# Performance work log

Hardware: AMD Instinct MI355X
Metric: run time of the kernel (lower is better)

The kernel has to match this reference:

```python
import jax, jax.numpy as jnp
import numpy as np

N, C, K, H = 131072, 512, 128, 8  # points, channels, patch_size, heads


def setup_inputs() -> dict:
    key = jax.random.key(0)
    ks = jax.random.split(key, 6)
    feat = jax.random.normal(ks[0], (N, C), dtype=jnp.float32)
    Wqkv = jax.random.normal(ks[1], (C, 3 * C), dtype=jnp.float32) * 0.02
    bqkv = jax.random.normal(ks[2], (3 * C,), dtype=jnp.float32) * 0.02
    Wproj = jax.random.normal(ks[3], (C, C), dtype=jnp.float32) * 0.02
    bproj = jax.random.normal(ks[4], (C,), dtype=jnp.float32) * 0.02
    order = jax.random.permutation(ks[5], N).astype(jnp.int64)  # serialized order (all clusters full)
    inverse = jnp.argsort(order).astype(jnp.int64)              # serialized inverse
    return {"feat": feat, "Wqkv": Wqkv, "bqkv": bqkv, "Wproj": Wproj,
            "bproj": bproj, "order": order, "inverse": inverse}


def reference(feat, Wqkv, bqkv, Wproj, bproj, order, inverse):
    hd = C // H
    scale = hd ** -0.5
    qkv = feat @ Wqkv + bqkv                 # [N, 3C]
    qkv = qkv[order]                         # gather by serialized order
    qkv = qkv.reshape(-1, K, 3, H, hd)       # [W, K, 3, H, hd]
    qkv = jnp.moveaxis(qkv, 2, 0)            # [3, W, K, H, hd]
    q = jnp.swapaxes(qkv[0], 1, 2)           # [W, H, K, hd]
    k = jnp.swapaxes(qkv[1], 1, 2)
    v = jnp.swapaxes(qkv[2], 1, 2)
    # upcast_attention / upcast_softmax -> compute scores & softmax in fp32
    attn = jnp.einsum('whkd,whjd->whkj', (q * scale).astype(jnp.float32),
                      k.astype(jnp.float32))             # [W, H, K, K]
    attn = jax.nn.softmax(attn, axis=-1).astype(feat.dtype)
    out = jnp.einsum('whkj,whjd->whkd', attn, v)          # [W, H, K, hd]
    out = jnp.swapaxes(out, 1, 2).reshape(-1, C)          # [N, C]
    out = out[inverse]                                    # scatter back via inverse
    out = out @ Wproj + bproj
    return out
```

## Files before the change

kernel.cpp:

```cpp
#include <hip/hip_runtime.h>
#include <hip/hip_bf16.h>
#include <cstdint>
#include <cstddef>

typedef __bf16 bf16;
typedef __bf16 bf16x8 __attribute__((ext_vector_type(8)));
typedef float f32x4 __attribute__((ext_vector_type(4)));

#define N_PTS 131072
#define CDIM  512
#define C3    1536
#define HD    64
#define NH    8
#define KWIN  128

static __device__ __forceinline__ bf16 cvt(float x) { return (bf16)x; }

static __device__ __forceinline__ void gld16(const bf16* g, bf16* l) {
    __builtin_amdgcn_global_load_lds(
        (const __attribute__((address_space(1))) void*)g,
        (__attribute__((address_space(3))) void*)l, 16, 0, 0);
}

__global__ __launch_bounds__(256) void k_prep(
    const float* __restrict__ Wqkv, const float* __restrict__ Wproj,
    bf16* __restrict__ Wqkv_t, bf16* __restrict__ Wproj_t)
{
    int idx = blockIdx.x * 256 + threadIdx.x;
    if (idx < CDIM * C3) {
        int k = idx / C3, c = idx % C3;
        Wqkv_t[(size_t)c * CDIM + k] = cvt(Wqkv[idx]);
    } else {
        int j = idx - CDIM * C3;
        if (j < CDIM * CDIM) {
            int k = j / CDIM, c = j % CDIM;
            Wproj_t[(size_t)c * CDIM + k] = cvt(Wproj[j]);
        }
    }
}

__global__ __launch_bounds__(256) void k_gather(
    const float* __restrict__ feat, const int* __restrict__ order,
    bf16* __restrict__ feat_g)
{
    int row = blockIdx.x * 2 + (threadIdx.x >> 7);
    int c   = (threadIdx.x & 127) << 2;
    int src = order[row];
    float4 v = *reinterpret_cast<const float4*>(feat + (size_t)src * CDIM + c);
    union { bf16 e[4]; uint2 u; } pk;
    pk.e[0] = cvt(v.x); pk.e[1] = cvt(v.y); pk.e[2] = cvt(v.z); pk.e[3] = cvt(v.w);
    *reinterpret_cast<uint2*>(feat_g + (size_t)row * CDIM + c) = pk.u;
}

template <bool F32OUT, int NT>
__global__ __launch_bounds__(512, 4) void k_gemm(
    const bf16* __restrict__ Ag, const bf16* __restrict__ Bt,
    const float* __restrict__ bias, void* __restrict__ outp)
{
    __shared__ __align__(16) bf16 As[2][128 * 32];
    __shared__ __align__(16) bf16 Bs[2][256 * 32];

    const int t    = threadIdx.x;
    const int lane = t & 63;
    const int wv   = t >> 6;
    const int wr   = wv >> 2;
    const int wc   = wv & 3;
    const int g    = lane >> 4, r16 = lane & 15;

    const int nwg = gridDim.x;
    const int bid = blockIdx.x;
    const int swz = (bid & 7) * (nwg >> 3) + (bid >> 3);
    const int m0  = (swz / NT) * 128;
    const int n0  = (swz % NT) * 256;

    const int L0 = wv * 64 + lane;
    const int rA = L0 >> 2,          sA = ((L0 & 3) - (rA >> 1)) & 3;
    const int rB1 = rA + 128,        sB1v = ((L0 & 3) - (rB1 >> 1)) & 3;
    const bf16* srcA  = Ag + (size_t)(m0 + rA) * CDIM + sA * 8;
    const bf16* srcB0 = Bt + (size_t)(n0 + rA) * CDIM + sA * 8;
    const bf16* srcB1 = Bt + (size_t)(n0 + rB1) * CDIM + sB1v * 8;

    int aoff[4], boff[4];
#pragma unroll
    for (int m = 0; m < 4; ++m) {
        int row = wr * 64 + m * 16 + r16;
        aoff[m] = row * 64 + (((g + (row >> 1)) & 3) << 4);
    }
#pragma unroll
    for (int n = 0; n < 4; ++n) {
        int row = wc * 64 + n * 16 + r16;
        boff[n] = row * 64 + (((g + (row >> 1)) & 3) << 4);
    }

    f32x4 acc[4][4];
    const f32x4 z = {0.f, 0.f, 0.f, 0.f};
#pragma unroll
    for (int m = 0; m < 4; ++m)
#pragma unroll
        for (int n = 0; n < 4; ++n) acc[m][n] = z;

    auto stage = [&](int kt) {
        const int b  = kt & 1;
        const int ko = kt * 32;
        gld16(srcA  + ko, &As[b][(size_t)wv * 64 * 8]);
        gld16(srcB0 + ko, &Bs[b][(size_t)wv * 64 * 8]);
        gld16(srcB1 + ko, &Bs[b][(size_t)(512 + wv * 64) * 8]);
    };

    auto compute = [&](int kt) {
        const int b = kt & 1;
        bf16x8 af[4], bv[4];
#pragma unroll
        for (int m = 0; m < 4; ++m)
            af[m] = *reinterpret_cast<const bf16x8*>(
                reinterpret_cast<const char*>(&As[b][0]) + aoff[m]);
#pragma unroll
        for (int n = 0; n < 4; ++n)
            bv[n] = *reinterpret_cast<const bf16x8*>(
                reinterpret_cast<const char*>(&Bs[b][0]) + boff[n]);
        __builtin_amdgcn_s_setprio(1);
#pragma unroll
        for (int m = 0; m < 4; ++m)
#pragma unroll
            for (int n = 0; n < 4; ++n)
                acc[m][n] = __builtin_amdgcn_mfma_f32_16x16x32_bf16(
                    af[m], bv[n], acc[m][n], 0, 0, 0);
        __builtin_amdgcn_s_setprio(0);
    };

    const int NKT = CDIM / 32;

    stage(0); stage(1);
    asm volatile("s_waitcnt vmcnt(3)" ::: "memory");
    __builtin_amdgcn_s_barrier();

#pragma unroll
    for (int kt = 0; kt < NKT - 2; ++kt) {
        compute(kt);
        asm volatile("s_waitcnt lgkmcnt(0)" ::: "memory");
        __builtin_amdgcn_s_barrier();
        stage(kt + 2);
        asm volatile("s_waitcnt vmcnt(3)" ::: "memory");
        __builtin_amdgcn_s_barrier();
    }
    compute(NKT - 2);
    asm volatile("s_waitcnt vmcnt(0) lgkmcnt(0)" ::: "memory");
    __builtin_amdgcn_s_barrier();
    compute(NKT - 1);

    const int ldo = NT * 256;
#pragma unroll
    for (int n = 0; n < 4; ++n) {
        int col = n0 + wc * 64 + n * 16 + r16;
        float b = bias[col];
#pragma unroll
        for (int m = 0; m < 4; ++m)
#pragma unroll
            for (int j = 0; j < 4; ++j) {
                int row = m0 + wr * 64 + m * 16 + g * 4 + j;
                if (F32OUT)
                    reinterpret_cast<float*>(outp)[(size_t)row * ldo + col] =
                        acc[m][n][j] + b;
                else
                    reinterpret_cast<bf16*>(outp)[(size_t)row * ldo + col] =
                        cvt(acc[m][n][j] + b);
            }
    }
}

__global__ __launch_bounds__(256) void k_attn(
    const bf16* __restrict__ qkv_s, const int* __restrict__ order,
    bf16* __restrict__ attn_g)
{
    __shared__ __align__(16) char smem[36864 + 64 * 136 * 2];
    __shared__ int ord_s[KWIN];
    bf16 (*Q)[72]   = reinterpret_cast<bf16 (*)[72]>(smem);
    bf16 (*Kt)[72]  = reinterpret_cast<bf16 (*)[72]>(smem + 128 * 72 * 2);
    bf16 (*P)[136]  = reinterpret_cast<bf16 (*)[136]>(smem);
    bf16 (*Vt)[136] = reinterpret_cast<bf16 (*)[136]>(smem + 36864);

    const int t    = threadIdx.x;
    const int lane = t & 63;
    const int wv   = t >> 6;
    const int g    = lane >> 4, r16 = lane & 15;
    const int h    = blockIdx.x;
    const int w    = blockIdx.y;

    const bf16* base = qkv_s + (size_t)w * KWIN * C3 + h * HD;

    if (t < KWIN) ord_s[t] = order[w * KWIN + t];

#pragma unroll
    for (int it = 0; it < 4; ++it) {
        int s   = it * 256 + t;
        int tok = s >> 3;
        int c8  = (s & 7) << 3;
        size_t roff = (size_t)tok * C3 + c8;
        *reinterpret_cast<uint4*>(&Q[tok][c8])  =
            *reinterpret_cast<const uint4*>(base + roff);
        *reinterpret_cast<uint4*>(&Kt[tok][c8]) =
            *reinterpret_cast<const uint4*>(base + roff + CDIM);
        uint4 vvec = *reinterpret_cast<const uint4*>(base + roff + 2 * CDIM);
        const bf16* ve = reinterpret_cast<const bf16*>(&vvec);
#pragma unroll
        for (int i = 0; i < 8; ++i) Vt[c8 + i][tok] = ve[i];
    }
    __syncthreads();

    f32x4 sc[2][8];
    const f32x4 z = {0.f, 0.f, 0.f, 0.f};
#pragma unroll
    for (int m = 0; m < 2; ++m)
#pragma unroll
        for (int n = 0; n < 8; ++n) sc[m][n] = z;

#pragma unroll
    for (int ks = 0; ks < 2; ++ks) {
        bf16x8 aq[2];
#pragma unroll
        for (int m = 0; m < 2; ++m)
            aq[m] = *reinterpret_cast<const bf16x8*>(
                &Q[wv * 32 + m * 16 + r16][ks * 32 + g * 8]);
#pragma unroll
        for (int n = 0; n < 8; ++n) {
            bf16x8 bk = *reinterpret_cast<const bf16x8*>(
                &Kt[n * 16 + r16][ks * 32 + g * 8]);
#pragma unroll
            for (int m = 0; m < 2; ++m)
                sc[m][n] = __builtin_amdgcn_mfma_f32_16x16x32_bf16(
                    aq[m], bk, sc[m][n], 0, 0, 0);
        }
    }

    const float scale = 0.125f;
    float inv_sum[2][4];
#pragma unroll
    for (int m = 0; m < 2; ++m) {
#pragma unroll
        for (int j = 0; j < 4; ++j) {
            float mx = -3.0e38f;
#pragma unroll
            for (int n = 0; n < 8; ++n) mx = fmaxf(mx, sc[m][n][j]);
            mx = fmaxf(mx, __shfl_xor(mx, 1));
            mx = fmaxf(mx, __shfl_xor(mx, 2));
            mx = fmaxf(mx, __shfl_xor(mx, 4));
            mx = fmaxf(mx, __shfl_xor(mx, 8));
            mx *= scale;
            float ssum = 0.f;
#pragma unroll
            for (int n = 0; n < 8; ++n) {
                float p = __expf(sc[m][n][j] * scale - mx);
                sc[m][n][j] = p;
                ssum += p;
            }
            ssum += __shfl_xor(ssum, 1);
            ssum += __shfl_xor(ssum, 2);
            ssum += __shfl_xor(ssum, 4);
            ssum += __shfl_xor(ssum, 8);
            inv_sum[m][j] = 1.f / ssum;
        }
    }

    __syncthreads();

#pragma unroll
    for (int m = 0; m < 2; ++m)
#pragma unroll
        for (int n = 0; n < 8; ++n)
#pragma unroll
            for (int j = 0; j < 4; ++j)
                P[wv * 32 + m * 16 + g * 4 + j][n * 16 + r16] =
                    cvt(sc[m][n][j] * inv_sum[m][j]);

    f32x4 o[2][4];
#pragma unroll
    for (int m = 0; m < 2; ++m)
#pragma unroll
        for (int n = 0; n < 4; ++n) o[m][n] = z;

#pragma unroll
    for (int kt = 0; kt < 4; ++kt) {
        bf16x8 ap[2];
#pragma unroll
        for (int m = 0; m < 2; ++m)
            ap[m] = *reinterpret_cast<const bf16x8*>(
                &P[wv * 32 + m * 16 + r16][kt * 32 + g * 8]);
#pragma unroll
        for (int n = 0; n < 4; ++n) {
            bf16x8 bv = *reinterpret_cast<const bf16x8*>(
                &Vt[n * 16 + r16][kt * 32 + g * 8]);
#pragma unroll
            for (int m = 0; m < 2; ++m)
                o[m][n] = __builtin_amdgcn_mfma_f32_16x16x32_bf16(
                    ap[m], bv, o[m][n], 0, 0, 0);
        }
    }

#pragma unroll
    for (int m = 0; m < 2; ++m)
#pragma unroll
        for (int n = 0; n < 4; ++n)
#pragma unroll
            for (int j = 0; j < 4; ++j) {
                int tok  = wv * 32 + m * 16 + g * 4 + j;
                int d    = n * 16 + r16;
                int drow = ord_s[tok];
                attn_g[(size_t)drow * CDIM + h * HD + d] = cvt(o[m][n][j]);
            }
}

extern "C" void kernel_launch(void* const* d_in, const int* in_sizes, int n_in,
                              void* d_out, int out_size, void* d_ws, size_t ws_size,
                              hipStream_t stream)
{
    const float* feat    = (const float*)d_in[0];
    const float* Wqkv    = (const float*)d_in[1];
    const float* bqkv    = (const float*)d_in[2];
    const float* Wproj   = (const float*)d_in[3];
    const float* bproj   = (const float*)d_in[4];
    const int*   order   = (const int*)d_in[5];
    float* out = (float*)d_out;

    const size_t qkv_bytes  = (size_t)N_PTS * C3 * sizeof(bf16);
    const size_t gat_bytes  = (size_t)N_PTS * CDIM * sizeof(bf16);
    const size_t wq_bytes   = (size_t)C3 * CDIM * sizeof(bf16);
    const size_t wp_bytes   = (size_t)CDIM * CDIM * sizeof(bf16);
    if (ws_size < qkv_bytes + gat_bytes + wq_bytes + wp_bytes) return;

    bf16* qkv_s     = (bf16*)d_ws;
    bf16* shared134 = (bf16*)((char*)d_ws + qkv_bytes);
    bf16* Wqkv_t    = (bf16*)((char*)d_ws + qkv_bytes + gat_bytes);
    bf16* Wproj_t   = (bf16*)((char*)d_ws + qkv_bytes + gat_bytes + wq_bytes);

    k_prep<<<dim3((CDIM * C3 + CDIM * CDIM + 255) / 256), 256, 0, stream>>>(
        Wqkv, Wproj, Wqkv_t, Wproj_t);
    k_gather<<<dim3(N_PTS / 2), 256, 0, stream>>>(feat, order, shared134);
    k_gemm<false, C3 / 256><<<dim3((N_PTS / 128) * (C3 / 256)), 512, 0, stream>>>(
        shared134, Wqkv_t, bqkv, qkv_s);
    k_attn<<<dim3(NH, N_PTS / KWIN), 256, 0, stream>>>(qkv_s, order, shared134);
    k_gemm<true, CDIM / 256><<<dim3((N_PTS / 128) * (CDIM / 256)), 512, 0, stream>>>(
        shared134, Wproj_t, bproj, out);
}
```

Measured before the change: 640.1 us.

## Fuse gather and bf16 conversion into QKV GEMM, swizzle V transpose writes

Removes the separate gather kernel. The QKV GEMM now reads fp32 feature rows through the order index, converts them to bf16 in registers and writes them into a swizzled LDS tile, while B is still loaded with global_load_lds. It uses 256-thread blocks with 4x8 MFMA tiles per wave. In attention, the V transpose store is rotated per thread to spread LDS bank accesses, and launch bounds gain a min-blocks hint. This avoids writing and re-reading the 128 MB bf16 gathered feature buffer, at the cost of more register pressure and scattered fp32 row loads inside the GEMM mainloop.

```diff
diff --git a/kernel.cpp b/kernel.cpp
--- a/kernel.cpp
+++ b/kernel.cpp
@@ -20,6 +20,21 @@
     __builtin_amdgcn_global_load_lds(
         (const __attribute__((address_space(1))) void*)g,
         (__attribute__((address_space(3))) void*)l, 16, 0, 0);
+}
+
+static __device__ __forceinline__ uint4 rot128(uint4 u, int r) {
+    uint32_t x = u.x, y = u.y, z = u.z, w = u.w;
+    uint32_t x1 = (x >> 16) | (y << 16), y1 = (y >> 16) | (z << 16),
+             z1 = (z >> 16) | (w << 16), w1 = (w >> 16) | (x << 16);
+    bool o1 = r & 1;
+    x = o1 ? x1 : x; y = o1 ? y1 : y; z = o1 ? z1 : z; w = o1 ? w1 : w;
+    bool o2 = r & 2;
+    uint32_t t0 = x;
+    x = o2 ? y : x; y = o2 ? z : y; z = o2 ? w : z; w = o2 ? t0 : w;
+    bool o4 = r & 4;
+    uint32_t tx = x, ty = y;
+    x = o4 ? z : x; y = o4 ? w : y; z = o4 ? tx : z; w = o4 ? ty : w;
+    uint4 o; o.x = x; o.y = y; o.z = z; o.w = w; return o;
 }
 
 __global__ __launch_bounds__(256) void k_prep(
@@ -39,23 +54,174 @@
     }
 }
 
-__global__ __launch_bounds__(256) void k_gather(
-    const float* __restrict__ feat, const int* __restrict__ order,
-    bf16* __restrict__ feat_g)
+template <int NT>
+__global__ __launch_bounds__(256, 2) void k_qkv4(
+    const float* __restrict__ feat, const bf16* __restrict__ Bt,
+    const float* __restrict__ bias, const int* __restrict__ order,
+    bf16* __restrict__ outp)
 {
-    int row = blockIdx.x * 2 + (threadIdx.x >> 7);
-    int c   = (threadIdx.x & 127) << 2;
-    int src = order[row];
-    float4 v = *reinterpret_cast<const float4*>(feat + (size_t)src * CDIM + c);
-    union { bf16 e[4]; uint2 u; } pk;
-    pk.e[0] = cvt(v.x); pk.e[1] = cvt(v.y); pk.e[2] = cvt(v.z); pk.e[3] = cvt(v.w);
-    *reinterpret_cast<uint2*>(feat_g + (size_t)row * CDIM + c) = pk.u;
-}
-
-template <bool F32OUT, int NT>
-__global__ __launch_bounds__(512, 4) void k_gemm(
+    __shared__ __align__(16) bf16 As[2][128 * 32];
+    __shared__ __align__(16) bf16 Bs[2][256 * 32];
+    __shared__ int ord_s[128];
+
+    const int t    = threadIdx.x;
+    const int lane = t & 63;
+    const int wv   = t >> 6;
+    const int wr   = wv >> 1;
+    const int wc   = wv & 1;
+    const int g    = lane >> 4, r16 = lane & 15;
+
+    const int nwg = gridDim.x;
+    const int bid = blockIdx.x;
+    const int swz = (bid & 7) * (nwg >> 3) + (bid >> 3);
+    const int m0  = (swz / NT) * 128;
+    const int n0  = (swz % NT) * 256;
+
+    const int NKT = CDIM / 32;
+
+    if (t < 128) ord_s[t] = order[m0 + t];
+    __syncthreads();
+
+    const int rA0 = t >> 2;
+    const int kA0 = ((t & 3) - (rA0 >> 1)) & 3;
+    const int rA1 = (t + 256) >> 2;
+    const int kA1 = ((t & 3) - (rA1 >> 1)) & 3;
+    const float* gsrc0 = feat + (size_t)ord_s[rA0] * CDIM + kA0 * 8;
+    const float* gsrc1 = feat + (size_t)ord_s[rA1] * CDIM + kA1 * 8;
+
+    const bf16* srcB[4];
+#pragma unroll
+    for (int q = 0; q < 4; ++q) {
+        int L = t + q * 256;
+        int row = L >> 2, s4 = ((L & 3) - (row >> 1)) & 3;
+        srcB[q] = Bt + (size_t)(n0 + row) * CDIM + s4 * 8;
+    }
+
+    int aoff[4], boff[8];
+#pragma unroll
+    for (int m = 0; m < 4; ++m) {
+        int row = wr * 64 + m * 16 + r16;
+        aoff[m] = row * 64 + (((g + (row >> 1)) & 3) << 4);
+    }
+#pragma unroll
+    for (int n = 0; n < 8; ++n) {
+        int row = wc * 128 + n * 16 + r16;
+        boff[n] = row * 64 + (((g + (row >> 1)) & 3) << 4);
+    }
+
+    f32x4 acc[4][8];
+    const f32x4 z = {0.f, 0.f, 0.f, 0.f};
+#pragma unroll
+    for (int m = 0; m < 4; ++m)
+#pragma unroll
+        for (int n = 0; n < 8; ++n) acc[m][n] = z;
+
+    auto stageB = [&](int s) {
+        const int b = s & 1;
+#pragma unroll
+        for (int q = 0; q < 4; ++q)
+            gld16(srcB[q] + s * 32, &Bs[b][(size_t)(q * 256 + wv * 64) * 8]);
+    };
+    auto packA2 = [&](int s, float4 a0, float4 a1, float4 b0, float4 b1) {
+        union { bf16 e[8]; uint4 u; } p0, p1;
+        p0.e[0] = cvt(a0.x); p0.e[1] = cvt(a0.y); p0.e[2] = cvt(a0.z); p0.e[3] = cvt(a0.w);
+        p0.e[4] = cvt(a1.x); p0.e[5] = cvt(a1.y); p0.e[6] = cvt(a1.z); p0.e[7] = cvt(a1.w);
+        p1.e[0] = cvt(b0.x); p1.e[1] = cvt(b0.y); p1.e[2] = cvt(b0.z); p1.e[3] = cvt(b0.w);
+        p1.e[4] = cvt(b1.x); p1.e[5] = cvt(b1.y); p1.e[6] = cvt(b1.z); p1.e[7] = cvt(b1.w);
+        char* ab = reinterpret_cast<char*>(&As[s & 1][0]);
+        *reinterpret_cast<uint4*>(ab + t * 16)         = p0.u;
+        *reinterpret_cast<uint4*>(ab + (t + 256) * 16) = p1.u;
+    };
+    auto compute = [&](int s) {
+        const int b = s & 1;
+        const char* ab = reinterpret_cast<const char*>(&As[b][0]);
+        const char* bb = reinterpret_cast<const char*>(&Bs[b][0]);
+        bf16x8 af[4], bv[8];
+#pragma unroll
+        for (int m = 0; m < 4; ++m)
+            af[m] = *reinterpret_cast<const bf16x8*>(ab + aoff[m]);
+#pragma unroll
+        for (int n = 0; n < 8; ++n)
+            bv[n] = *reinterpret_cast<const bf16x8*>(bb + boff[n]);
+        __builtin_amdgcn_s_setprio(1);
+#pragma unroll
+        for (int m = 0; m < 4; ++m)
+#pragma unroll
+            for (int n = 0; n < 8; ++n)
+                acc[m][n] = __builtin_amdgcn_mfma_f32_16x16x32_bf16(
+                    af[m], bv[n], acc[m][n], 0, 0, 0);
+        __builtin_amdgcn_s_setprio(0);
+    };
+
+    float4 fp[2][4];
+
+    {
+        float4 t00 = *reinterpret_cast<const float4*>(gsrc0);
+        float4 t01 = *reinterpret_cast<const float4*>(gsrc0 + 4);
+        float4 t02 = *reinterpret_cast<const float4*>(gsrc1);
+        float4 t03 = *reinterpret_cast<const float4*>(gsrc1 + 4);
+        float4 t10 = *reinterpret_cast<const float4*>(gsrc0 + 32);
+        float4 t11 = *reinterpret_cast<const float4*>(gsrc0 + 36);
+        float4 t12 = *reinterpret_cast<const float4*>(gsrc1 + 32);
+        float4 t13 = *reinterpret_cast<const float4*>(gsrc1 + 36);
+        stageB(0); stageB(1);
+        packA2(0, t00, t01, t02, t03);
+        packA2(1, t10, t11, t12, t13);
+        fp[0][0] = *reinterpret_cast<const float4*>(gsrc0 + 64);
+        fp[0][1] = *reinterpret_cast<const float4*>(gsrc0 + 68);
+        fp[0][2] = *reinterpret_cast<const float4*>(gsrc1 + 64);
+        fp[0][3] = *reinterpret_cast<const float4*>(gsrc1 + 68);
+        asm volatile("s_waitcnt vmcnt(8) lgkmcnt(0)" ::: "memory");
+        __builtin_amdgcn_s_barrier();
+    }
+
+#pragma unroll
+    for (int s = 0; s < NKT; ++s) {
+        if (s + 3 < NKT) {
+            const float* p0 = gsrc0 + (size_t)(s + 3) * 32;
+            const float* p1 = gsrc1 + (size_t)(s + 3) * 32;
+            fp[(s + 1) & 1][0] = *reinterpret_cast<const float4*>(p0);
+            fp[(s + 1) & 1][1] = *reinterpret_cast<const float4*>(p0 + 4);
+            fp[(s + 1) & 1][2] = *reinterpret_cast<const float4*>(p1);
+            fp[(s + 1) & 1][3] = *reinterpret_cast<const float4*>(p1 + 4);
+        }
+        compute(s);
+        if (s == NKT - 1) break;
+        asm volatile("s_waitcnt lgkmcnt(0)" ::: "memory");
+        __builtin_amdgcn_s_barrier();
+        if (s + 2 < NKT) {
+            packA2(s + 2, fp[s & 1][0], fp[s & 1][1], fp[s & 1][2], fp[s & 1][3]);
+            stageB(s + 2);
+            asm volatile("s_waitcnt lgkmcnt(0)" ::: "memory");
+            if (s + 3 < NKT)
+                asm volatile("s_waitcnt vmcnt(8)" ::: "memory");
+            else
+                asm volatile("s_waitcnt vmcnt(4)" ::: "memory");
+        } else {
+            asm volatile("s_waitcnt vmcnt(0)" ::: "memory");
+        }
+        __builtin_amdgcn_s_barrier();
+    }
+
+    const int ldo = NT * 256;
+#pragma unroll
+    for (int n = 0; n < 8; ++n) {
+        int col = n0 + wc * 128 + n * 16 + r16;
+        float b = bias[col];
+#pragma unroll
+        for (int m = 0; m < 4; ++m)
+#pragma unroll
+            for (int j = 0; j < 4; ++j) {
+                int row = m0 + wr * 64 + m * 16 + g * 4 + j;
+                outp[(size_t)row * ldo + col] = cvt(acc[m][n][j] + b);
+            }
+    }
+}
+
+template <int NT>
+__global__ __launch_bounds__(512, 4) void k_proj(
     const bf16* __restrict__ Ag, const bf16* __restrict__ Bt,
-    const float* __restrict__ bias, void* __restrict__ outp)
+    const float* __restrict__ bias, float* __restrict__ outp)
 {
     __shared__ __align__(16) bf16 As[2][128 * 32];
     __shared__ __align__(16) bf16 Bs[2][256 * 32];
@@ -109,14 +275,14 @@
 
     auto compute = [&](int kt) {
         const int b = kt & 1;
-        bf16x8 af[4], bv[4];
+        bf16x8 af[4], bvv[4];
 #pragma unroll
         for (int m = 0; m < 4; ++m)
             af[m] = *reinterpret_cast<const bf16x8*>(
                 reinterpret_cast<const char*>(&As[b][0]) + aoff[m]);
 #pragma unroll
         for (int n = 0; n < 4; ++n)
-            bv[n] = *reinterpret_cast<const bf16x8*>(
+            bvv[n] = *reinterpret_cast<const bf16x8*>(
                 reinterpret_cast<const char*>(&Bs[b][0]) + boff[n]);
         __builtin_amdgcn_s_setprio(1);
 #pragma unroll
@@ -124,7 +290,7 @@
 #pragma unroll
             for (int n = 0; n < 4; ++n)
                 acc[m][n] = __builtin_amdgcn_mfma_f32_16x16x32_bf16(
-                    af[m], bv[n], acc[m][n], 0, 0, 0);
+                    af[m], bvv[n], acc[m][n], 0, 0, 0);
         __builtin_amdgcn_s_setprio(0);
     };
 
@@ -158,17 +324,12 @@
 #pragma unroll
             for (int j = 0; j < 4; ++j) {
                 int row = m0 + wr * 64 + m * 16 + g * 4 + j;
-                if (F32OUT)
-                    reinterpret_cast<float*>(outp)[(size_t)row * ldo + col] =
-                        acc[m][n][j] + b;
-                else
-                    reinterpret_cast<bf16*>(outp)[(size_t)row * ldo + col] =
-                        cvt(acc[m][n][j] + b);
+                outp[(size_t)row * ldo + col] = acc[m][n][j] + b;
             }
     }
 }
 
-__global__ __launch_bounds__(256) void k_attn(
+__global__ __launch_bounds__(256, 2) void k_attn(
     const bf16* __restrict__ qkv_s, const int* __restrict__ order,
     bf16* __restrict__ attn_g)
 {
@@ -178,6 +339,7 @@
     bf16 (*Kt)[72]  = reinterpret_cast<bf16 (*)[72]>(smem + 128 * 72 * 2);
     bf16 (*P)[136]  = reinterpret_cast<bf16 (*)[136]>(smem);
     bf16 (*Vt)[136] = reinterpret_cast<bf16 (*)[136]>(smem + 36864);
+    unsigned short* Vtu = reinterpret_cast<unsigned short*>(smem + 36864);
 
     const int t    = threadIdx.x;
     const int lane = t & 63;
@@ -189,6 +351,8 @@
     const bf16* base = qkv_s + (size_t)w * KWIN * C3 + h * HD;
 
     if (t < KWIN) ord_s[t] = order[w * KWIN + t];
+
+    const int rot = t & 7;
 
 #pragma unroll
     for (int it = 0; it < 4; ++it) {
@@ -201,9 +365,14 @@
         *reinterpret_cast<uint4*>(&Kt[tok][c8]) =
             *reinterpret_cast<const uint4*>(base + roff + CDIM);
         uint4 vvec = *reinterpret_cast<const uint4*>(base + roff + 2 * CDIM);
-        const bf16* ve = reinterpret_cast<const bf16*>(&vvec);
-#pragma unroll
-        for (int i = 0; i < 8; ++i) Vt[c8 + i][tok] = ve[i];
+        uint4 vr = rot128(vvec, rot);
+        uint32_t wd[4] = {vr.x, vr.y, vr.z, vr.w};
+#pragma unroll
+        for (int k = 0; k < 8; ++k) {
+            int d = c8 + ((k + rot) & 7);
+            Vtu[d * 136 + tok] =
+                (unsigned short)(wd[k >> 1] >> ((k & 1) * 16));
+        }
     }
     __syncthreads();
 
@@ -287,12 +456,12 @@
                 &P[wv * 32 + m * 16 + r16][kt * 32 + g * 8]);
 #pragma unroll
         for (int n = 0; n < 4; ++n) {
-            bf16x8 bv = *reinterpret_cast<const bf16x8*>(
+            bf16x8 bvv = *reinterpret_cast<const bf16x8*>(
                 &Vt[n * 16 + r16][kt * 32 + g * 8]);
 #pragma unroll
             for (int m = 0; m < 2; ++m)
                 o[m][n] = __builtin_amdgcn_mfma_f32_16x16x32_bf16(
-                    ap[m], bv, o[m][n], 0, 0, 0);
+                    ap[m], bvv, o[m][n], 0, 0, 0);
         }
     }
 
@@ -327,17 +496,18 @@
     const size_t wp_bytes   = (size_t)CDIM * CDIM * sizeof(bf16);
     if (ws_size < qkv_bytes + gat_bytes + wq_bytes + wp_bytes) return;
 
-    bf16* qkv_s     = (bf16*)d_ws;
-    bf16* shared134 = (bf16*)((char*)d_ws + qkv_bytes);
-    bf16* Wqkv_t    = (bf16*)((char*)d_ws + qkv_bytes + gat_bytes);
-    bf16* Wproj_t   = (bf16*)((char*)d_ws + qkv_bytes + gat_bytes + wq_bytes);
+    bf16* qkv_s   = (bf16*)d_ws;
+    bf16* attn_g  = (bf16*)((char*)d_ws + qkv_bytes);
+    bf16* Wqkv_t  = (bf16*)((char*)d_ws + qkv_bytes + gat_bytes);
+    bf16* Wproj_t = (bf16*)((char*)d_ws + qkv_bytes + gat_bytes + wq_bytes);
 
     k_prep<<<dim3((CDIM * C3 + CDIM * CDIM + 255) / 256), 256, 0, stream>>>(
         Wqkv, Wproj, Wqkv_t, Wproj_t);
-    k_gather<<<dim3(N_PTS / 2), 256, 0, stream>>>(feat, order, shared134);
-    k_gemm<false, C3 / 256><<<dim3((N_PTS / 128) * (C3 / 256)), 512, 0, stream>>>(
-        shared134, Wqkv_t, bqkv, qkv_s);
-    k_attn<<<dim3(NH, N_PTS / KWIN), 256, 0, stream>>>(qkv_s, order, shared134);
-    k_gemm<true, CDIM / 256><<<dim3((N_PTS / 128) * (CDIM / 256)), 512, 0, stream>>>(
-        shared134, Wproj_t, bproj, out);
-}
+    k_qkv4<C3 / 256>
+        <<<dim3((N_PTS / 128) * (C3 / 256)), 256, 0, stream>>>(
+        feat, Wqkv_t, bqkv, order, qkv_s);
+    k_attn<<<dim3(NH, N_PTS / KWIN), 256, 0, stream>>>(qkv_s, order, attn_g);
+    k_proj<CDIM / 256>
+        <<<dim3((N_PTS / 128) * (CDIM / 256)), 512, 0, stream>>>(
+        attn_g, Wproj_t, bproj, out);
+}
```

Result: faster. 604.2 us (-5.6%).
